# Kernel optimization log

Hardware: AMD Instinct MI355X
Metric: run time of the kernel (lower is better)

Reference implementation:

```python
import jax, jax.numpy as jnp
import numpy as np

B, C, N = 8, 128, 65536
NUM_OBJ = 64


def setup_inputs() -> dict:
    key = jax.random.key(0)
    k1, k2 = jax.random.split(key)
    point_features = jax.random.normal(k1, (B, C, N), dtype=jnp.float32)
    # box assignment per point (output of points_in_boxes_gpu in the original)
    box_idx = jax.random.randint(k2, (B, N), 0, NUM_OBJ, dtype=jnp.int64)
    return {"point_features": point_features, "box_idx": box_idx, "num_obj": NUM_OBJ}


def reference(point_features, box_idx, num_obj):
    # point_features: (B, C, N) float; box_idx: (B, N) int in [0, num_obj)
    b, c, n = point_features.shape
    # (B, N, C) -> (B*N, C): one feature row per point
    feats = jnp.transpose(point_features, (0, 2, 1)).reshape(b * n, c)
    # global segment id: batch-local boxes become distinct segments
    seg_ids = (jnp.arange(b, dtype=box_idx.dtype)[:, None] * num_obj + box_idx).reshape(-1)
    # fused gather + segment max (replaces per-box max_pool1d python loop)
    seg_max = jax.ops.segment_max(feats, seg_ids, num_segments=b * num_obj)
    # guard (empty segments -> -inf); original assumes nonempty boxes
    seg_max = jnp.where(jnp.isfinite(seg_max), seg_max, jnp.zeros_like(seg_max))
    return seg_max  # (B*num_obj, C) == pretext_head_feats
```

## Files before the change

kernel.cpp:

```cpp
#include <hip/hip_runtime.h>
#include <cstdint>
#include <cstddef>

#define BATCH 8
#define CH    128
#define NPTS  65536
#define NOBJ  64
#define TPB   256
#define SEGEL (CH * NOBJ)

__device__ __forceinline__ uint32_t enc_f32(float f) {
    uint32_t x = __float_as_uint(f);
    return x ^ ((uint32_t)((int32_t)x >> 31) | 0x80000000u);
}
__device__ __forceinline__ float dec_f32(uint32_t u) {
    uint32_t x = u ^ ((uint32_t)((int32_t)(~u) >> 31) | 0x80000000u);
    return __uint_as_float(x);
}

template <int NCHUNK>
__global__ __launch_bounds__(TPB) void seg_max_ws(
        const float* __restrict__ pf,
        const int*   __restrict__ bidx,
        uint32_t*    __restrict__ ws)
{
    constexpr int PPB = NPTS / NCHUNK;
    constexpr int J   = PPB / 4 / 32;
    static_assert(J >= 1, "chunk too small");

    __shared__ uint32_t acc[SEGEL];

    const int tid  = threadIdx.x;
    const int wave = tid >> 6;
    const int lane = tid & 63;
    const int cl   = lane >> 3;
    const int pq   = lane & 7;

    const int b     = blockIdx.x / NCHUNK;
    const int chunk = blockIdx.x % NCHUNK;
    const int n0    = chunk * PPB;

    for (int i = tid; i < SEGEL; i += TPB) acc[i] = 0u;

    int s[J][4];
    #pragma unroll
    for (int j = 0; j < J; ++j) {
        const int q = j * 32 + wave * 8 + pq;
        const int4 sv = *(const int4*)(bidx + (size_t)b * NPTS + n0 + q * 4);
        s[j][0] = sv.x ^ cl;  s[j][1] = sv.y ^ cl;
        s[j][2] = sv.z ^ cl;  s[j][3] = sv.w ^ cl;
    }
    __syncthreads();

    const float* pbase = pf + (size_t)b * CH * NPTS + n0;
    const int qoff = (wave * 8 + pq) * 4;

    float4 v[J], vn[J];
    {
        const float* pc = pbase + (size_t)cl * NPTS;
        #pragma unroll
        for (int j = 0; j < J; ++j) v[j] = *(const float4*)(pc + j * 128 + qoff);
    }

    for (int cb = 0; cb < CH; cb += 8) {
        if (cb + 8 < CH) {
            const float* pn = pbase + (size_t)(cb + 8 + cl) * NPTS;
            #pragma unroll
            for (int j = 0; j < J; ++j) vn[j] = *(const float4*)(pn + j * 128 + qoff);
        }
        uint32_t* row = acc + (cb + cl) * NOBJ;
        #pragma unroll
        for (int j = 0; j < J; ++j) {
            atomicMax(&row[s[j][0]], enc_f32(v[j].x));
            atomicMax(&row[s[j][1]], enc_f32(v[j].y));
            atomicMax(&row[s[j][2]], enc_f32(v[j].z));
            atomicMax(&row[s[j][3]], enc_f32(v[j].w));
        }
        #pragma unroll
        for (int j = 0; j < J; ++j) v[j] = vn[j];
    }
    __syncthreads();

    uint32_t* wsb = ws + (size_t)blockIdx.x * SEGEL;
    for (int e = tid; e < SEGEL; e += TPB) wsb[e] = acc[e];
}

template <int NCHUNK>
__global__ __launch_bounds__(256) void reduce_ws(
        const uint32_t* __restrict__ ws, float* __restrict__ out)
{
    const int g = blockIdx.x * 256 + threadIdx.x;
    const int b = g >> 13;
    const int e = g & (SEGEL - 1);
    const uint32_t* p = ws + (size_t)b * NCHUNK * SEGEL + e;
    uint32_t m = 0u;
    #pragma unroll
    for (int k = 0; k < NCHUNK; ++k) m = max(m, p[(size_t)k * SEGEL]);
    const int c   = e >> 6;
    const int seg = (e & 63) ^ (c & 7);
    float f = 0.0f;
    if (m) { f = dec_f32(m); if (!isfinite(f)) f = 0.0f; }
    out[(size_t)(b * NOBJ + seg) * CH + c] = f;
}

__global__ __launch_bounds__(256) void init_out_kernel(uint32_t* __restrict__ out, int n) {
    int i = blockIdx.x * blockDim.x + threadIdx.x;
    if (i < n) out[i] = 0u;
}

__global__ __launch_bounds__(TPB) void seg_max_atomic(
        const float* __restrict__ pf, const int* __restrict__ bidx,
        uint32_t* __restrict__ out)
{
    constexpr int PPB = 1024;
    __shared__ uint32_t acc[SEGEL];
    const int tid   = threadIdx.x;
    const int b     = blockIdx.x / (NPTS / PPB);
    const int chunk = blockIdx.x % (NPTS / PPB);
    const int n0    = chunk * PPB;
    for (int i = tid; i < SEGEL; i += TPB) acc[i] = 0u;
    __syncthreads();
    const int4 sv = *(const int4*)(bidx + (size_t)b * NPTS + n0 + tid * 4);
    const float* p = pf + (size_t)b * CH * NPTS + n0 + tid * 4;
    uint32_t* row = acc;
    #pragma unroll 4
    for (int c = 0; c < CH; ++c, p += NPTS, row += NOBJ) {
        const float4 v = *(const float4*)p;
        atomicMax(&row[sv.x], enc_f32(v.x));
        atomicMax(&row[sv.y], enc_f32(v.y));
        atomicMax(&row[sv.z], enc_f32(v.z));
        atomicMax(&row[sv.w], enc_f32(v.w));
    }
    __syncthreads();
    for (int e = tid; e < SEGEL; e += TPB) {
        const int seg = e & (NOBJ - 1);
        const int c   = e >> 6;
        const uint32_t v = acc[c * NOBJ + seg];
        if (v) atomicMax(&out[(size_t)(b * NOBJ + seg) * CH + c], v);
    }
}

__global__ __launch_bounds__(256) void finalize_kernel(uint32_t* __restrict__ out, int n) {
    int i = blockIdx.x * blockDim.x + threadIdx.x;
    if (i >= n) return;
    const uint32_t u = out[i];
    float f = 0.0f;
    if (u) { f = dec_f32(u); if (!isfinite(f)) f = 0.0f; }
    ((float*)out)[i] = f;
}

extern "C" void kernel_launch(void* const* d_in, const int* in_sizes, int n_in,
                              void* d_out, int out_size, void* d_ws, size_t ws_size,
                              hipStream_t stream) {
    const float* pf   = (const float*)d_in[0];
    const int*   bidx = (const int*)d_in[1];

    const size_t need128 = (size_t)BATCH * 128 * SEGEL * 4;
    const size_t need64  = (size_t)BATCH *  64 * SEGEL * 4;

    if (ws_size >= need128) {
        uint32_t* ws = (uint32_t*)d_ws;
        seg_max_ws<128><<<BATCH * 128, TPB, 0, stream>>>(pf, bidx, ws);
        reduce_ws<128><<<(BATCH * SEGEL) / 256, 256, 0, stream>>>(ws, (float*)d_out);
    } else if (ws_size >= need64) {
        uint32_t* ws = (uint32_t*)d_ws;
        seg_max_ws<64><<<BATCH * 64, TPB, 0, stream>>>(pf, bidx, ws);
        reduce_ws<64><<<(BATCH * SEGEL) / 256, 256, 0, stream>>>(ws, (float*)d_out);
    } else {
        uint32_t* out = (uint32_t*)d_out;
        init_out_kernel<<<(out_size + 255) / 256, 256, 0, stream>>>(out, out_size);
        seg_max_atomic<<<BATCH * (NPTS / 1024), TPB, 0, stream>>>(pf, bidx, out);
        finalize_kernel<<<(out_size + 255) / 256, 256, 0, stream>>>(out, out_size);
    }
}
```

Before: 367.2 us.

## Deepen channel prefetch, widen blocks, halve chunks, vectorize workspace reduce

The segment-max kernel now keeps two channel groups in flight in a fully unrolled double buffer, runs 512 threads per block with 64 chunks instead of 128, and requests an occupancy of 4 through launch bounds. The LDS zeroing and workspace writeback use uint4 accesses, and the reduce kernel handles four elements per thread with vector loads over half as many partials. The aim is to hide global-load latency better and to cut workspace traffic and reduce work. In exchange, more registers per thread may limit occupancy, and the 128-chunk path is removed.

```diff
diff --git a/kernel.cpp b/kernel.cpp
--- a/kernel.cpp
+++ b/kernel.cpp
@@ -6,7 +6,6 @@
 #define CH    128
 #define NPTS  65536
 #define NOBJ  64
-#define TPB   256
 #define SEGEL (CH * NOBJ)
 
 __device__ __forceinline__ uint32_t enc_f32(float f) {
@@ -18,15 +17,16 @@
     return __uint_as_float(x);
 }
 
-template <int NCHUNK>
-__global__ __launch_bounds__(TPB) void seg_max_ws(
+template <int NCHUNK, int TPB>
+__global__ __launch_bounds__(TPB, 4) void seg_max_ws(
         const float* __restrict__ pf,
         const int*   __restrict__ bidx,
         uint32_t*    __restrict__ ws)
 {
     constexpr int PPB = NPTS / NCHUNK;
-    constexpr int J   = PPB / 4 / 32;
-    static_assert(J >= 1, "chunk too small");
+    constexpr int QPP = TPB / 8;
+    constexpr int J   = PPB / (QPP * 4);
+    static_assert(J >= 1 && PPB % (QPP * 4) == 0, "bad geometry");
 
     __shared__ uint32_t acc[SEGEL];
 
@@ -40,12 +40,13 @@
     const int chunk = blockIdx.x % NCHUNK;
     const int n0    = chunk * PPB;
 
-    for (int i = tid; i < SEGEL; i += TPB) acc[i] = 0u;
+    for (int i = tid; i < SEGEL / 4; i += TPB)
+        ((uint4*)acc)[i] = make_uint4(0u, 0u, 0u, 0u);
 
     int s[J][4];
     #pragma unroll
     for (int j = 0; j < J; ++j) {
-        const int q = j * 32 + wave * 8 + pq;
+        const int q = j * QPP + wave * 8 + pq;
         const int4 sv = *(const int4*)(bidx + (size_t)b * NPTS + n0 + q * 4);
         s[j][0] = sv.x ^ cl;  s[j][1] = sv.y ^ cl;
         s[j][2] = sv.z ^ cl;  s[j][3] = sv.w ^ cl;
@@ -55,52 +56,64 @@
     const float* pbase = pf + (size_t)b * CH * NPTS + n0;
     const int qoff = (wave * 8 + pq) * 4;
 
-    float4 v[J], vn[J];
-    {
-        const float* pc = pbase + (size_t)cl * NPTS;
-        #pragma unroll
-        for (int j = 0; j < J; ++j) v[j] = *(const float4*)(pc + j * 128 + qoff);
-    }
+    float4 buf[2][J];
+    #pragma unroll
+    for (int j = 0; j < J; ++j)
+        buf[0][j] = *(const float4*)(pbase + (size_t)cl * NPTS + j * (QPP * 4) + qoff);
+    #pragma unroll
+    for (int j = 0; j < J; ++j)
+        buf[1][j] = *(const float4*)(pbase + (size_t)(8 + cl) * NPTS + j * (QPP * 4) + qoff);
 
-    for (int cb = 0; cb < CH; cb += 8) {
-        if (cb + 8 < CH) {
-            const float* pn = pbase + (size_t)(cb + 8 + cl) * NPTS;
-            #pragma unroll
-            for (int j = 0; j < J; ++j) vn[j] = *(const float4*)(pn + j * 128 + qoff);
-        }
+    #pragma unroll
+    for (int ci = 0; ci < CH / 8; ++ci) {
+        const int cb = ci * 8;
         uint32_t* row = acc + (cb + cl) * NOBJ;
+        float4* cur = buf[ci & 1];
         #pragma unroll
         for (int j = 0; j < J; ++j) {
-            atomicMax(&row[s[j][0]], enc_f32(v[j].x));
-            atomicMax(&row[s[j][1]], enc_f32(v[j].y));
-            atomicMax(&row[s[j][2]], enc_f32(v[j].z));
-            atomicMax(&row[s[j][3]], enc_f32(v[j].w));
+            atomicMax(&row[s[j][0]], enc_f32(cur[j].x));
+            atomicMax(&row[s[j][1]], enc_f32(cur[j].y));
+            atomicMax(&row[s[j][2]], enc_f32(cur[j].z));
+            atomicMax(&row[s[j][3]], enc_f32(cur[j].w));
         }
-        #pragma unroll
-        for (int j = 0; j < J; ++j) v[j] = vn[j];
+        if (ci + 2 < CH / 8) {
+            const float* pn = pbase + (size_t)(cb + 16 + cl) * NPTS;
+            #pragma unroll
+            for (int j = 0; j < J; ++j)
+                cur[j] = *(const float4*)(pn + j * (QPP * 4) + qoff);
+        }
     }
     __syncthreads();
 
-    uint32_t* wsb = ws + (size_t)blockIdx.x * SEGEL;
-    for (int e = tid; e < SEGEL; e += TPB) wsb[e] = acc[e];
+    uint4* wsb = (uint4*)(ws + (size_t)blockIdx.x * SEGEL);
+    for (int e = tid; e < SEGEL / 4; e += TPB) wsb[e] = ((const uint4*)acc)[e];
 }
 
 template <int NCHUNK>
-__global__ __launch_bounds__(256) void reduce_ws(
+__global__ __launch_bounds__(64) void reduce_ws(
         const uint32_t* __restrict__ ws, float* __restrict__ out)
 {
-    const int g = blockIdx.x * 256 + threadIdx.x;
-    const int b = g >> 13;
-    const int e = g & (SEGEL - 1);
-    const uint32_t* p = ws + (size_t)b * NCHUNK * SEGEL + e;
-    uint32_t m = 0u;
+    const int g  = blockIdx.x * 64 + threadIdx.x;
+    const int b  = g >> 11;
+    const int e4 = (g & 2047) * 4;
+    const uint4* p = (const uint4*)(ws + (size_t)b * NCHUNK * SEGEL + e4);
+    uint4 m = make_uint4(0u, 0u, 0u, 0u);
+    #pragma unroll 16
+    for (int k = 0; k < NCHUNK; ++k) {
+        const uint4 v = p[(size_t)k * (SEGEL / 4)];
+        m.x = max(m.x, v.x); m.y = max(m.y, v.y);
+        m.z = max(m.z, v.z); m.w = max(m.w, v.w);
+    }
+    const int c   = e4 >> 6;
+    const int sw0 = e4 & 63;
+    const uint32_t mv[4] = {m.x, m.y, m.z, m.w};
     #pragma unroll
-    for (int k = 0; k < NCHUNK; ++k) m = max(m, p[(size_t)k * SEGEL]);
-    const int c   = e >> 6;
-    const int seg = (e & 63) ^ (c & 7);
-    float f = 0.0f;
-    if (m) { f = dec_f32(m); if (!isfinite(f)) f = 0.0f; }
-    out[(size_t)(b * NOBJ + seg) * CH + c] = f;
+    for (int i = 0; i < 4; ++i) {
+        const int seg = (sw0 + i) ^ (c & 7);
+        float f = 0.0f;
+        if (mv[i]) { f = dec_f32(mv[i]); if (!isfinite(f)) f = 0.0f; }
+        out[(size_t)(b * NOBJ + seg) * CH + c] = f;
+    }
 }
 
 __global__ __launch_bounds__(256) void init_out_kernel(uint32_t* __restrict__ out, int n) {
@@ -108,7 +121,7 @@
     if (i < n) out[i] = 0u;
 }
 
-__global__ __launch_bounds__(TPB) void seg_max_atomic(
+__global__ __launch_bounds__(256) void seg_max_atomic(
         const float* __restrict__ pf, const int* __restrict__ bidx,
         uint32_t* __restrict__ out)
 {
@@ -118,7 +131,7 @@
     const int b     = blockIdx.x / (NPTS / PPB);
     const int chunk = blockIdx.x % (NPTS / PPB);
     const int n0    = chunk * PPB;
-    for (int i = tid; i < SEGEL; i += TPB) acc[i] = 0u;
+    for (int i = tid; i < SEGEL; i += 256) acc[i] = 0u;
     __syncthreads();
     const int4 sv = *(const int4*)(bidx + (size_t)b * NPTS + n0 + tid * 4);
     const float* p = pf + (size_t)b * CH * NPTS + n0 + tid * 4;
@@ -132,7 +145,7 @@
         atomicMax(&row[sv.w], enc_f32(v.w));
     }
     __syncthreads();
-    for (int e = tid; e < SEGEL; e += TPB) {
+    for (int e = tid; e < SEGEL; e += 256) {
         const int seg = e & (NOBJ - 1);
         const int c   = e >> 6;
         const uint32_t v = acc[c * NOBJ + seg];
@@ -155,21 +168,16 @@
     const float* pf   = (const float*)d_in[0];
     const int*   bidx = (const int*)d_in[1];
 
-    const size_t need128 = (size_t)BATCH * 128 * SEGEL * 4;
-    const size_t need64  = (size_t)BATCH *  64 * SEGEL * 4;
+    const size_t need64 = (size_t)BATCH * 64 * SEGEL * 4;
 
-    if (ws_size >= need128) {
+    if (ws_size >= need64) {
         uint32_t* ws = (uint32_t*)d_ws;
-        seg_max_ws<128><<<BATCH * 128, TPB, 0, stream>>>(pf, bidx, ws);
-        reduce_ws<128><<<(BATCH * SEGEL) / 256, 256, 0, stream>>>(ws, (float*)d_out);
-    } else if (ws_size >= need64) {
-        uint32_t* ws = (uint32_t*)d_ws;
-        seg_max_ws<64><<<BATCH * 64, TPB, 0, stream>>>(pf, bidx, ws);
-        reduce_ws<64><<<(BATCH * SEGEL) / 256, 256, 0, stream>>>(ws, (float*)d_out);
+        seg_max_ws<64, 512><<<BATCH * 64, 512, 0, stream>>>(pf, bidx, ws);
+        reduce_ws<64><<<256, 64, 0, stream>>>(ws, (float*)d_out);
     } else {
         uint32_t* out = (uint32_t*)d_out;
         init_out_kernel<<<(out_size + 255) / 256, 256, 0, stream>>>(out, out_size);
-        seg_max_atomic<<<BATCH * (NPTS / 1024), TPB, 0, stream>>>(pf, bidx, out);
+        seg_max_atomic<<<BATCH * (NPTS / 1024), 256, 0, stream>>>(pf, bidx, out);
         finalize_kernel<<<(out_size + 255) / 256, 256, 0, stream>>>(out, out_size);
     }
 }
```

Result: no change. 370.6 us (+0.9%).
